# Kernel optimization log

Measured on AMD Instinct MI355X. Metric: run time of the kernel, lower is better.

## Reference

```python
import jax, jax.numpy as jnp
import numpy as np

HID = 512
POOL = 4096
N_OBJ = 1280
N_REL = 16384
NUM_OBJ_CLS = 151
NUM_REL_CLS = 51


def setup_inputs() -> dict:
    key = jax.random.key(0)
    ks = jax.random.split(key, 12)
    return {
        'edge_ctx': jax.random.normal(ks[0], (N_OBJ, HID), dtype=jnp.float32),
        'union_features': jax.random.normal(ks[1], (N_REL, POOL), dtype=jnp.float32),
        'W_post_emb': jax.random.normal(ks[2], (HID, 2 * HID), dtype=jnp.float32) * (10.0 / np.sqrt(HID)),
        'b_post_emb': jax.random.normal(ks[3], (2 * HID,), dtype=jnp.float32) * 0.01,
        'W_post_cat': jax.random.normal(ks[4], (2 * HID, POOL), dtype=jnp.float32) * 0.02,
        'b_post_cat': jnp.zeros((POOL,), dtype=jnp.float32),
        'W_rel': jax.random.normal(ks[5], (POOL, NUM_REL_CLS), dtype=jnp.float32) * 0.02,
        'b_rel': jnp.zeros((NUM_REL_CLS,), dtype=jnp.float32),
        'freq_table': jax.random.normal(ks[6], (NUM_OBJ_CLS * NUM_OBJ_CLS, NUM_REL_CLS), dtype=jnp.float32),
        'pair_idx': jax.random.randint(ks[7], (N_REL, 2), 0, N_OBJ, dtype=jnp.int32),
        'obj_preds': jax.random.randint(ks[8], (N_OBJ,), 0, NUM_OBJ_CLS, dtype=jnp.int32),
    }


def reference(edge_ctx, union_features, W_post_emb, b_post_emb, W_post_cat,
              b_post_cat, W_rel, b_rel, freq_table, pair_idx, obj_preds):
    # post_emb: [N_obj, 2*hid]; view(N,2,hid) -> head = first hid, tail = last hid
    edge_rep = edge_ctx @ W_post_emb + b_post_emb
    head_rep = edge_rep[:, :HID]   # [N_obj, hid]
    tail_rep = edge_rep[:, HID:]   # [N_obj, hid]

    # gather subject/object reps per relation pair, concat -> [N_rel, 2*hid]
    prod_rep = jnp.concatenate(
        (head_rep[pair_idx[:, 0]], tail_rep[pair_idx[:, 1]]), axis=-1)

    prod_rep = prod_rep @ W_post_cat + b_post_cat        # [N_rel, pool]
    prod_rep = prod_rep * union_features                  # use_vision fuse
    rel_dists = prod_rep @ W_rel + b_rel                  # [N_rel, num_rel]

    # frequency bias: Embedding over [num_obj^2, num_rel] indexed by label pair
    bias_idx = obj_preds[pair_idx[:, 0]] * NUM_OBJ_CLS + obj_preds[pair_idx[:, 1]]
    rel_dists = rel_dists + freq_table[bias_idx]
    return rel_dists
```

## Files before the change

kernel.cpp:

```cpp
#include <hip/hip_runtime.h>

#define HID 512
#define POOL 4096
#define N_OBJ 1280
#define N_REL 16384
#define NOC 151
#define NRC 51
#define KSPLIT 8

typedef _Float16 half_t;
typedef half_t h16x8 __attribute__((ext_vector_type(8)));
typedef float f32x4 __attribute__((ext_vector_type(4)));

#define LDSTR 72

__device__ __forceinline__ void kt_tile(
    const float* __restrict__ src, half_t* __restrict__ dst,
    int K, int N, int kb, int nb, half_t* Ts)
{
    const int t = threadIdx.x;
    const int kr = t >> 4;
    const int nc = (t & 15) * 4;
#pragma unroll
    for (int p = 0; p < 4; ++p) {
        float4 v = *(const float4*)(src + (size_t)(kb + kr + 16 * p) * N + nb + nc);
        Ts[(nc + 0) * LDSTR + kr + 16 * p] = (half_t)v.x;
        Ts[(nc + 1) * LDSTR + kr + 16 * p] = (half_t)v.y;
        Ts[(nc + 2) * LDSTR + kr + 16 * p] = (half_t)v.z;
        Ts[(nc + 3) * LDSTR + kr + 16 * p] = (half_t)v.w;
    }
    __syncthreads();
    const int n = t >> 2, kk = (t & 3) * 16;
    half_t* d = dst + (size_t)(nb + n) * K + kb + kk;
    *(h16x8*)(d)     = *(const h16x8*)&Ts[n * LDSTR + kk];
    *(h16x8*)(d + 8) = *(const h16x8*)&Ts[n * LDSTR + kk + 8];
}

__global__ __launch_bounds__(256) void k_prep(
    const float* __restrict__ We, const float* __restrict__ Wc,
    const float* __restrict__ Wrel,
    half_t* __restrict__ Wet, half_t* __restrict__ Wct, half_t* __restrict__ Wt)
{
    __shared__ __align__(16) char smem[64 * NRC * 4];
    const int b = blockIdx.x;
    if (b < 1024) {
        kt_tile(Wc, Wct, 1024, POOL, (b & 15) * 64, (b >> 4) * 64, (half_t*)smem);
    } else if (b < 1152) {
        const int c = b - 1024;
        kt_tile(We, Wet, HID, 1024, (c & 7) * 64, (c >> 3) * 64, (half_t*)smem);
    } else {
        float* Ls = (float*)smem;
        const int kb = (b - 1152) * 64;
        const int t = threadIdx.x;
        for (int f = t; f < 64 * NRC; f += 256)
            Ls[f] = Wrel[(size_t)kb * NRC + f];
        __syncthreads();
        const int n = t >> 2, kc = t & 3;
        h16x8 o0, o1;
#pragma unroll
        for (int e = 0; e < 8; ++e) {
            o0[e] = (n < NRC) ? (half_t)Ls[(kc * 16 + e) * NRC + n] : (half_t)0.0f;
            o1[e] = (n < NRC) ? (half_t)Ls[(kc * 16 + 8 + e) * NRC + n] : (half_t)0.0f;
        }
        half_t* d = Wt + (size_t)n * POOL + kb + kc * 16;
        *(h16x8*)(d)     = o0;
        *(h16x8*)(d + 8) = o1;
    }
}

__global__ __launch_bounds__(256) void k1_edge_rep(
    const float* __restrict__ edge_ctx,
    const half_t* __restrict__ Wet,
    const float* __restrict__ be,
    half_t* __restrict__ E)
{
    __shared__ __align__(16) half_t As[64 * LDSTR];
    __shared__ __align__(16) half_t Bs[64 * LDSTR];

    const int m0 = blockIdx.x * 64;
    const int n0 = blockIdx.y * 64;
    const int t = threadIdx.x;
    const int wave = t >> 6, lane = t & 63;
    const int quad = lane >> 4, l16 = lane & 15;

    const int ar  = t >> 2;
    const int akb = (t & 3) * 16;

    f32x4 acc[4] = {};

    for (int k0 = 0; k0 < HID; k0 += 64) {
        {
            const float* src = edge_ctx + (size_t)(m0 + ar) * HID + k0 + akb;
#pragma unroll
            for (int i = 0; i < 2; ++i) {
                float4 va = *(const float4*)(src + 8 * i);
                float4 vb = *(const float4*)(src + 8 * i + 4);
                h16x8 o;
                o[0] = (half_t)va.x; o[1] = (half_t)va.y;
                o[2] = (half_t)va.z; o[3] = (half_t)va.w;
                o[4] = (half_t)vb.x; o[5] = (half_t)vb.y;
                o[6] = (half_t)vb.z; o[7] = (half_t)vb.w;
                *(h16x8*)&As[ar * LDSTR + akb + 8 * i] = o;
            }
        }
        {
            const half_t* src = Wet + (size_t)(n0 + ar) * HID + k0 + akb;
            *(h16x8*)&Bs[ar * LDSTR + akb]     = *(const h16x8*)(src);
            *(h16x8*)&Bs[ar * LDSTR + akb + 8] = *(const h16x8*)(src + 8);
        }
        __syncthreads();
#pragma unroll
        for (int s = 0; s < 2; ++s) {
            h16x8 a = *(const h16x8*)&As[(wave * 16 + l16) * LDSTR + s * 32 + quad * 8];
#pragma unroll
            for (int nt = 0; nt < 4; ++nt) {
                h16x8 b = *(const h16x8*)&Bs[(nt * 16 + l16) * LDSTR + s * 32 + quad * 8];
                acc[nt] = __builtin_amdgcn_mfma_f32_16x16x32_f16(a, b, acc[nt], 0, 0, 0);
            }
        }
        __syncthreads();
    }
#pragma unroll
    for (int nt = 0; nt < 4; ++nt) {
        int n = n0 + nt * 16 + l16;
        float bias = be[n];
#pragma unroll
        for (int r = 0; r < 4; ++r) {
            int m = m0 + wave * 16 + quad * 4 + r;
            E[(size_t)m * 1024 + n] = (half_t)(acc[nt][r] + bias);
        }
    }
}

__global__ __launch_bounds__(256) void k2_ht(
    const half_t* __restrict__ E,
    const half_t* __restrict__ Wct,
    const float* __restrict__ bcat,
    half_t* __restrict__ Hws,
    half_t* __restrict__ Tws)
{
    __shared__ __align__(16) half_t As[128 * LDSTR];
    __shared__ __align__(16) half_t Bs[128 * LDSTR];

    const int z  = blockIdx.z;
    const int m0 = blockIdx.x * 128;
    const int n0 = blockIdx.y * 128;
    const int t = threadIdx.x;
    const int wave = t >> 6, lane = t & 63;
    const int quad = lane >> 4, l16 = lane & 15;
    const int wr = wave >> 1, wc = wave & 1;

    const int srow = t >> 3;
    const int sc   = (t & 7) * 8;

    f32x4 acc[4][4] = {};

    for (int k0 = 0; k0 < HID; k0 += 64) {
#pragma unroll
        for (int p = 0; p < 4; ++p) {
            int row = srow + 32 * p;
            *(h16x8*)&As[row * LDSTR + sc] =
                *(const h16x8*)(E + (size_t)(m0 + row) * 1024 + z * 512 + k0 + sc);
            *(h16x8*)&Bs[row * LDSTR + sc] =
                *(const h16x8*)(Wct + (size_t)(n0 + row) * 1024 + z * 512 + k0 + sc);
        }
        __syncthreads();
#pragma unroll
        for (int s = 0; s < 2; ++s) {
            h16x8 a[4], b[4];
#pragma unroll
            for (int i = 0; i < 4; ++i) {
                a[i] = *(const h16x8*)&As[(wr * 64 + i * 16 + l16) * LDSTR + s * 32 + quad * 8];
                b[i] = *(const h16x8*)&Bs[(wc * 64 + i * 16 + l16) * LDSTR + s * 32 + quad * 8];
            }
#pragma unroll
            for (int ri = 0; ri < 4; ++ri)
#pragma unroll
                for (int ci = 0; ci < 4; ++ci)
                    acc[ri][ci] = __builtin_amdgcn_mfma_f32_16x16x32_f16(
                        a[ri], b[ci], acc[ri][ci], 0, 0, 0);
        }
        __syncthreads();
    }
    half_t* outp = z ? Tws : Hws;
#pragma unroll
    for (int ci = 0; ci < 4; ++ci) {
        int n = n0 + wc * 64 + ci * 16 + l16;
        float bias = z ? 0.0f : bcat[n];
#pragma unroll
        for (int ri = 0; ri < 4; ++ri) {
#pragma unroll
            for (int r = 0; r < 4; ++r) {
                int m = m0 + wr * 64 + ri * 16 + quad * 4 + r;
                outp[(size_t)m * POOL + n] = (half_t)(acc[ri][ci][r] + bias);
            }
        }
    }
}

__global__ __launch_bounds__(256) void k3_main(
    const float* __restrict__ unionf,
    const half_t* __restrict__ Hws,
    const half_t* __restrict__ Tws,
    const half_t* __restrict__ Wt,
    const float* __restrict__ brel,
    const float* __restrict__ freq,
    const int* __restrict__ pair_idx,
    const int* __restrict__ obj_preds,
    float* __restrict__ out)
{
    __shared__ __align__(16) half_t As[64 * LDSTR];
    __shared__ __align__(16) half_t Bs[64 * LDSTR];

    const int R0 = blockIdx.x * 64;
    const int kbase = blockIdx.y * (POOL / KSPLIT);
    const int t = threadIdx.x;
    const int wave = t >> 6, lane = t & 63;
    const int quad = lane >> 4, l16 = lane & 15;

    const int ar  = t >> 2;
    const int akb = (t & 3) * 16;

    const int2 pr = *(const int2*)(pair_idx + 2 * (R0 + ar));
    const half_t* Hrow = Hws + (size_t)pr.x * POOL;
    const half_t* Trow = Tws + (size_t)pr.y * POOL;
    const float*  urow = unionf + (size_t)(R0 + ar) * POOL;

    f32x4 acc[4] = {};

    for (int k0 = kbase; k0 < kbase + POOL / KSPLIT; k0 += 64) {
#pragma unroll
        for (int i = 0; i < 2; ++i) {
            h16x8 hv = *(const h16x8*)(Hrow + k0 + akb + 8 * i);
            h16x8 tv = *(const h16x8*)(Trow + k0 + akb + 8 * i);
            float4 ua = *(const float4*)(urow + k0 + akb + 8 * i);
            float4 ub = *(const float4*)(urow + k0 + akb + 8 * i + 4);
            h16x8 o;
            o[0] = (half_t)(((float)hv[0] + (float)tv[0]) * ua.x);
            o[1] = (half_t)(((float)hv[1] + (float)tv[1]) * ua.y);
            o[2] = (half_t)(((float)hv[2] + (float)tv[2]) * ua.z);
            o[3] = (half_t)(((float)hv[3] + (float)tv[3]) * ua.w);
            o[4] = (half_t)(((float)hv[4] + (float)tv[4]) * ub.x);
            o[5] = (half_t)(((float)hv[5] + (float)tv[5]) * ub.y);
            o[6] = (half_t)(((float)hv[6] + (float)tv[6]) * ub.z);
            o[7] = (half_t)(((float)hv[7] + (float)tv[7]) * ub.w);
            *(h16x8*)&As[ar * LDSTR + akb + 8 * i] = o;
        }
        {
            const half_t* src = Wt + (size_t)ar * POOL + k0 + akb;
            *(h16x8*)&Bs[ar * LDSTR + akb]     = *(const h16x8*)(src);
            *(h16x8*)&Bs[ar * LDSTR + akb + 8] = *(const h16x8*)(src + 8);
        }
        __syncthreads();
#pragma unroll
        for (int s = 0; s < 2; ++s) {
            h16x8 a = *(const h16x8*)&As[(wave * 16 + l16) * LDSTR + s * 32 + quad * 8];
#pragma unroll
            for (int nt = 0; nt < 4; ++nt) {
                h16x8 b = *(const h16x8*)&Bs[(nt * 16 + l16) * LDSTR + s * 32 + quad * 8];
                acc[nt] = __builtin_amdgcn_mfma_f32_16x16x32_f16(a, b, acc[nt], 0, 0, 0);
            }
        }
        __syncthreads();
    }
    const bool first = (blockIdx.y == 0);
#pragma unroll
    for (int r = 0; r < 4; ++r) {
        int grow = R0 + wave * 16 + quad * 4 + r;
        const float* frow = nullptr;
        if (first) {
            int2 p = *(const int2*)(pair_idx + 2 * grow);
            frow = freq + (size_t)(obj_preds[p.x] * NOC + obj_preds[p.y]) * NRC;
        }
#pragma unroll
        for (int nt = 0; nt < 4; ++nt) {
            int n = nt * 16 + l16;
            if (n < NRC) {
                float v = acc[nt][r];
                if (first) v += brel[n] + frow[n];
                atomicAdd(&out[(size_t)grow * NRC + n], v);
            }
        }
    }
}

extern "C" void kernel_launch(void* const* d_in, const int* in_sizes, int n_in,
                              void* d_out, int out_size, void* d_ws, size_t ws_size,
                              hipStream_t stream) {
    const float* edge_ctx  = (const float*)d_in[0];
    const float* unionf    = (const float*)d_in[1];
    const float* We        = (const float*)d_in[2];
    const float* be        = (const float*)d_in[3];
    const float* Wc        = (const float*)d_in[4];
    const float* bcat      = (const float*)d_in[5];
    const float* Wrel      = (const float*)d_in[6];
    const float* brel      = (const float*)d_in[7];
    const float* freq      = (const float*)d_in[8];
    const int*   pair_idx  = (const int*)d_in[9];
    const int*   obj_preds = (const int*)d_in[10];
    float* out = (float*)d_out;

    char* ws = (char*)d_ws;
    half_t* E   = (half_t*)(ws);
    half_t* H   = (half_t*)(ws + 2621440);
    half_t* T   = (half_t*)(ws + 13107200);
    half_t* Wt  = (half_t*)(ws + 23592960);
    half_t* Wct = (half_t*)(ws + 24117248);
    half_t* Wet = (half_t*)(ws + 32505856);

    hipMemsetAsync(out, 0, (size_t)out_size * sizeof(float), stream);

    k_prep<<<1216, 256, 0, stream>>>(We, Wc, Wrel, Wet, Wct, Wt);
    k1_edge_rep<<<dim3(N_OBJ / 64, 1024 / 64), 256, 0, stream>>>(edge_ctx, Wet, be, E);
    k2_ht<<<dim3(N_OBJ / 128, POOL / 128, 2), 256, 0, stream>>>(E, Wct, bcat, H, T);
    k3_main<<<dim3(N_REL / 64, KSPLIT), 256, 0, stream>>>(unionf, H, T, Wt, brel, freq,
                                                          pair_idx, obj_preds, out);
}
```

Before: 459.9 us.

## Merge prep, edge-rep GEMM and output zeroing into one front kernel

Combines the weight-transpose prep kernel, the edge_ctx GEMM, and the output memset into a single launch with block-range dispatch. The edge GEMM now reads the fp32 W_post_emb directly and transposes it into LDS, so the separate Wet transpose pass is dropped. The union_features loads in the main kernel switch to nontemporal loads to avoid polluting cache with streamed data. This removes two launches and a memset, at the cost of a less regular mixed-role kernel and strided LDS stores for the transposed B tile.

```diff
diff --git a/kernel.cpp b/kernel.cpp
--- a/kernel.cpp
+++ b/kernel.cpp
@@ -36,22 +36,88 @@
     *(h16x8*)(d + 8) = *(const h16x8*)&Ts[n * LDSTR + kk + 8];
 }
 
-__global__ __launch_bounds__(256) void k_prep(
-    const float* __restrict__ We, const float* __restrict__ Wc,
+__global__ __launch_bounds__(256) void k_front(
+    const float* __restrict__ edge_ctx,
+    const float* __restrict__ We,
+    const float* __restrict__ be,
+    const float* __restrict__ Wc,
     const float* __restrict__ Wrel,
-    half_t* __restrict__ Wet, half_t* __restrict__ Wct, half_t* __restrict__ Wt)
+    half_t* __restrict__ E,
+    half_t* __restrict__ Wct,
+    half_t* __restrict__ Wt,
+    float* __restrict__ out)
 {
-    __shared__ __align__(16) char smem[64 * NRC * 4];
+    __shared__ __align__(16) char smem[2 * 64 * LDSTR * 2];
     const int b = blockIdx.x;
-    if (b < 1024) {
-        kt_tile(Wc, Wct, 1024, POOL, (b & 15) * 64, (b >> 4) * 64, (half_t*)smem);
-    } else if (b < 1152) {
-        const int c = b - 1024;
-        kt_tile(We, Wet, HID, 1024, (c & 7) * 64, (c >> 3) * 64, (half_t*)smem);
-    } else {
+    const int t = threadIdx.x;
+
+    if (b < 320) {
+        half_t* As = (half_t*)smem;
+        half_t* Bs = (half_t*)(smem + 64 * LDSTR * 2);
+
+        const int m0 = (b % 20) * 64;
+        const int n0 = (b / 20) * 64;
+        const int wave = t >> 6, lane = t & 63;
+        const int quad = lane >> 4, l16 = lane & 15;
+
+        const int ar  = t >> 2;
+        const int akb = (t & 3) * 16;
+        const int kr  = t >> 4;
+        const int nc  = (t & 15) * 4;
+
+        f32x4 acc[4] = {};
+
+        for (int k0 = 0; k0 < HID; k0 += 64) {
+            {
+                const float* src = edge_ctx + (size_t)(m0 + ar) * HID + k0 + akb;
+#pragma unroll
+                for (int i = 0; i < 2; ++i) {
+                    float4 va = *(const float4*)(src + 8 * i);
+                    float4 vb = *(const float4*)(src + 8 * i + 4);
+                    h16x8 o;
+                    o[0] = (half_t)va.x; o[1] = (half_t)va.y;
+                    o[2] = (half_t)va.z; o[3] = (half_t)va.w;
+                    o[4] = (half_t)vb.x; o[5] = (half_t)vb.y;
+                    o[6] = (half_t)vb.z; o[7] = (half_t)vb.w;
+                    *(h16x8*)&As[ar * LDSTR + akb + 8 * i] = o;
+                }
+            }
+#pragma unroll
+            for (int p = 0; p < 4; ++p) {
+                float4 v = *(const float4*)(We + (size_t)(k0 + kr + 16 * p) * 1024 + n0 + nc);
+                Bs[(nc + 0) * LDSTR + kr + 16 * p] = (half_t)v.x;
+                Bs[(nc + 1) * LDSTR + kr + 16 * p] = (half_t)v.y;
+                Bs[(nc + 2) * LDSTR + kr + 16 * p] = (half_t)v.z;
+                Bs[(nc + 3) * LDSTR + kr + 16 * p] = (half_t)v.w;
+            }
+            __syncthreads();
+#pragma unroll
+            for (int s = 0; s < 2; ++s) {
+                h16x8 a = *(const h16x8*)&As[(wave * 16 + l16) * LDSTR + s * 32 + quad * 8];
+#pragma unroll
+                for (int nt = 0; nt < 4; ++nt) {
+                    h16x8 bb = *(const h16x8*)&Bs[(nt * 16 + l16) * LDSTR + s * 32 + quad * 8];
+                    acc[nt] = __builtin_amdgcn_mfma_f32_16x16x32_f16(a, bb, acc[nt], 0, 0, 0);
+                }
+            }
+            __syncthreads();
+        }
+#pragma unroll
+        for (int nt = 0; nt < 4; ++nt) {
+            int n = n0 + nt * 16 + l16;
+            float bias = be[n];
+#pragma unroll
+            for (int r = 0; r < 4; ++r) {
+                int m = m0 + wave * 16 + quad * 4 + r;
+                E[(size_t)m * 1024 + n] = (half_t)(acc[nt][r] + bias);
+            }
+        }
+    } else if (b < 1344) {
+        const int c = b - 320;
+        kt_tile(Wc, Wct, 1024, POOL, (c & 15) * 64, (c >> 4) * 64, (half_t*)smem);
+    } else if (b < 1408) {
         float* Ls = (float*)smem;
-        const int kb = (b - 1152) * 64;
-        const int t = threadIdx.x;
+        const int kb = (b - 1344) * 64;
         for (int f = t; f < 64 * NRC; f += 256)
             Ls[f] = Wrel[(size_t)kb * NRC + f];
         __syncthreads();
@@ -65,70 +131,12 @@
         half_t* d = Wt + (size_t)n * POOL + kb + kc * 16;
         *(h16x8*)(d)     = o0;
         *(h16x8*)(d + 8) = o1;
-    }
-}
-
-__global__ __launch_bounds__(256) void k1_edge_rep(
-    const float* __restrict__ edge_ctx,
-    const half_t* __restrict__ Wet,
-    const float* __restrict__ be,
-    half_t* __restrict__ E)
-{
-    __shared__ __align__(16) half_t As[64 * LDSTR];
-    __shared__ __align__(16) half_t Bs[64 * LDSTR];
-
-    const int m0 = blockIdx.x * 64;
-    const int n0 = blockIdx.y * 64;
-    const int t = threadIdx.x;
-    const int wave = t >> 6, lane = t & 63;
-    const int quad = lane >> 4, l16 = lane & 15;
-
-    const int ar  = t >> 2;
-    const int akb = (t & 3) * 16;
-
-    f32x4 acc[4] = {};
-
-    for (int k0 = 0; k0 < HID; k0 += 64) {
-        {
-            const float* src = edge_ctx + (size_t)(m0 + ar) * HID + k0 + akb;
-#pragma unroll
-            for (int i = 0; i < 2; ++i) {
-                float4 va = *(const float4*)(src + 8 * i);
-                float4 vb = *(const float4*)(src + 8 * i + 4);
-                h16x8 o;
-                o[0] = (half_t)va.x; o[1] = (half_t)va.y;
-                o[2] = (half_t)va.z; o[3] = (half_t)va.w;
-                o[4] = (half_t)vb.x; o[5] = (half_t)vb.y;
-                o[6] = (half_t)vb.z; o[7] = (half_t)vb.w;
-                *(h16x8*)&As[ar * LDSTR + akb + 8 * i] = o;
-            }
-        }
-        {
-            const half_t* src = Wet + (size_t)(n0 + ar) * HID + k0 + akb;
-            *(h16x8*)&Bs[ar * LDSTR + akb]     = *(const h16x8*)(src);
-            *(h16x8*)&Bs[ar * LDSTR + akb + 8] = *(const h16x8*)(src + 8);
-        }
-        __syncthreads();
-#pragma unroll
-        for (int s = 0; s < 2; ++s) {
-            h16x8 a = *(const h16x8*)&As[(wave * 16 + l16) * LDSTR + s * 32 + quad * 8];
-#pragma unroll
-            for (int nt = 0; nt < 4; ++nt) {
-                h16x8 b = *(const h16x8*)&Bs[(nt * 16 + l16) * LDSTR + s * 32 + quad * 8];
-                acc[nt] = __builtin_amdgcn_mfma_f32_16x16x32_f16(a, b, acc[nt], 0, 0, 0);
-            }
-        }
-        __syncthreads();
-    }
-#pragma unroll
-    for (int nt = 0; nt < 4; ++nt) {
-        int n = n0 + nt * 16 + l16;
-        float bias = be[n];
-#pragma unroll
-        for (int r = 0; r < 4; ++r) {
-            int m = m0 + wave * 16 + quad * 4 + r;
-            E[(size_t)m * 1024 + n] = (half_t)(acc[nt][r] + bias);
-        }
+    } else {
+        f32x4 z = {0.0f, 0.0f, 0.0f, 0.0f};
+        f32x4* o4 = (f32x4*)out;
+        const int total = (N_REL * NRC) / 4;
+        for (int i = (b - 1408) * 256 + t; i < total; i += 64 * 256)
+            o4[i] = z;
     }
 }
 
@@ -167,18 +175,18 @@
         __syncthreads();
 #pragma unroll
         for (int s = 0; s < 2; ++s) {
-            h16x8 a[4], b[4];
+            h16x8 a[4], bfr[4];
 #pragma unroll
             for (int i = 0; i < 4; ++i) {
-                a[i] = *(const h16x8*)&As[(wr * 64 + i * 16 + l16) * LDSTR + s * 32 + quad * 8];
-                b[i] = *(const h16x8*)&Bs[(wc * 64 + i * 16 + l16) * LDSTR + s * 32 + quad * 8];
+                a[i]   = *(const h16x8*)&As[(wr * 64 + i * 16 + l16) * LDSTR + s * 32 + quad * 8];
+                bfr[i] = *(const h16x8*)&Bs[(wc * 64 + i * 16 + l16) * LDSTR + s * 32 + quad * 8];
             }
 #pragma unroll
             for (int ri = 0; ri < 4; ++ri)
 #pragma unroll
                 for (int ci = 0; ci < 4; ++ci)
                     acc[ri][ci] = __builtin_amdgcn_mfma_f32_16x16x32_f16(
-                        a[ri], b[ci], acc[ri][ci], 0, 0, 0);
+                        a[ri], bfr[ci], acc[ri][ci], 0, 0, 0);
         }
         __syncthreads();
     }
@@ -233,17 +241,17 @@
         for (int i = 0; i < 2; ++i) {
             h16x8 hv = *(const h16x8*)(Hrow + k0 + akb + 8 * i);
             h16x8 tv = *(const h16x8*)(Trow + k0 + akb + 8 * i);
-            float4 ua = *(const float4*)(urow + k0 + akb + 8 * i);
-            float4 ub = *(const float4*)(urow + k0 + akb + 8 * i + 4);
+            f32x4 ua = __builtin_nontemporal_load((const f32x4*)(urow + k0 + akb + 8 * i));
+            f32x4 ub = __builtin_nontemporal_load((const f32x4*)(urow + k0 + akb + 8 * i + 4));
             h16x8 o;
-            o[0] = (half_t)(((float)hv[0] + (float)tv[0]) * ua.x);
-            o[1] = (half_t)(((float)hv[1] + (float)tv[1]) * ua.y);
-            o[2] = (half_t)(((float)hv[2] + (float)tv[2]) * ua.z);
-            o[3] = (half_t)(((float)hv[3] + (float)tv[3]) * ua.w);
-            o[4] = (half_t)(((float)hv[4] + (float)tv[4]) * ub.x);
-            o[5] = (half_t)(((float)hv[5] + (float)tv[5]) * ub.y);
-            o[6] = (half_t)(((float)hv[6] + (float)tv[6]) * ub.z);
-            o[7] = (half_t)(((float)hv[7] + (float)tv[7]) * ub.w);
+            o[0] = (half_t)(((float)hv[0] + (float)tv[0]) * ua[0]);
+            o[1] = (half_t)(((float)hv[1] + (float)tv[1]) * ua[1]);
+            o[2] = (half_t)(((float)hv[2] + (float)tv[2]) * ua[2]);
+            o[3] = (half_t)(((float)hv[3] + (float)tv[3]) * ua[3]);
+            o[4] = (half_t)(((float)hv[4] + (float)tv[4]) * ub[0]);
+            o[5] = (half_t)(((float)hv[5] + (float)tv[5]) * ub[1]);
+            o[6] = (half_t)(((float)hv[6] + (float)tv[6]) * ub[2]);
+            o[7] = (half_t)(((float)hv[7] + (float)tv[7]) * ub[3]);
             *(h16x8*)&As[ar * LDSTR + akb + 8 * i] = o;
         }
         {
@@ -257,8 +265,8 @@
             h16x8 a = *(const h16x8*)&As[(wave * 16 + l16) * LDSTR + s * 32 + quad * 8];
 #pragma unroll
             for (int nt = 0; nt < 4; ++nt) {
-                h16x8 b = *(const h16x8*)&Bs[(nt * 16 + l16) * LDSTR + s * 32 + quad * 8];
-                acc[nt] = __builtin_amdgcn_mfma_f32_16x16x32_f16(a, b, acc[nt], 0, 0, 0);
+                h16x8 bb = *(const h16x8*)&Bs[(nt * 16 + l16) * LDSTR + s * 32 + quad * 8];
+                acc[nt] = __builtin_amdgcn_mfma_f32_16x16x32_f16(a, bb, acc[nt], 0, 0, 0);
             }
         }
         __syncthreads();
@@ -306,12 +314,8 @@
     half_t* T   = (half_t*)(ws + 13107200);
     half_t* Wt  = (half_t*)(ws + 23592960);
     half_t* Wct = (half_t*)(ws + 24117248);
-    half_t* Wet = (half_t*)(ws + 32505856);
-
-    hipMemsetAsync(out, 0, (size_t)out_size * sizeof(float), stream);
-
-    k_prep<<<1216, 256, 0, stream>>>(We, Wc, Wrel, Wet, Wct, Wt);
-    k1_edge_rep<<<dim3(N_OBJ / 64, 1024 / 64), 256, 0, stream>>>(edge_ctx, Wet, be, E);
+
+    k_front<<<1472, 256, 0, stream>>>(edge_ctx, We, be, Wc, Wrel, E, Wct, Wt, out);
     k2_ht<<<dim3(N_OBJ / 128, POOL / 128, 2), 256, 0, stream>>>(E, Wct, bcat, H, T);
     k3_main<<<dim3(N_REL / 64, KSPLIT), 256, 0, stream>>>(unionf, H, T, Wt, brel, freq,
                                                           pair_idx, obj_preds, out);
```

Result: slower. 471.2 us (+2.5%).
